# Kernel optimization log

Hardware: AMD Instinct MI355X
Metric: run time of the kernel (lower is better)

Reference implementation:

```python
import jax, jax.numpy as jnp
import numpy as np
from jax import lax

B, KLEN, KDIM, QDIM, ADIM, VDIM = 32, 2000, 512, 512, 512, 512
CONV_CH, CONV_K = 10, 201

def setup_inputs() -> dict:
    key = jax.random.key(0)
    ks = jax.random.split(key, 16)
    s = lambda fan: 1.0 / np.sqrt(fan)
    return {
        "key": jax.random.normal(ks[0], (B, KLEN, KDIM), jnp.float32),
        "value": jax.random.normal(ks[1], (B, KLEN, VDIM), jnp.float32),
        "query": jax.random.normal(ks[2], (B, 1, QDIM), jnp.float32),
        "aw_prev": jnp.zeros((B, 1, KLEN), jnp.float32),
        "mask": jnp.ones((B, 1, KLEN), jnp.int32),
        # parameters (torch nn.Linear: y = x @ W.T + b, W is [out,in])
        "Wk": jax.random.uniform(ks[3], (ADIM, KDIM), jnp.float32, -s(KDIM), s(KDIM)),
        "bk": jax.random.uniform(ks[4], (ADIM,), jnp.float32, -s(KDIM), s(KDIM)),
        "Wq": jax.random.uniform(ks[5], (ADIM, QDIM), jnp.float32, -s(QDIM), s(QDIM)),
        "conv_w": jax.random.uniform(ks[6], (CONV_CH, 1, CONV_K), jnp.float32, -s(CONV_K), s(CONV_K)),
        "Wconv": jax.random.uniform(ks[7], (ADIM, CONV_CH), jnp.float32, -s(CONV_CH), s(CONV_CH)),
        "v": jax.random.uniform(ks[8], (ADIM,), jnp.float32, -s(ADIM), s(ADIM)),
    }

def reference(key, value, query, aw_prev, mask, Wk, bk, Wq, conv_w, Wconv, v):
    # location-aware attention, qlen == 1, sharpening_factor == 1, no dropout (eval)
    kproj = jnp.einsum('bkd,ad->bka', key, Wk) + bk              # [B, klen, adim]
    qproj = jnp.einsum('bqd,ad->bqa', query, Wq)                 # [B, 1, adim]
    # conv over previous attention weights: 1D 'same' conv, 1 -> CONV_CH channels
    conv_feat = lax.conv_general_dilated(
        aw_prev, conv_w, window_strides=(1,), padding='SAME',
        dimension_numbers=('NCH', 'OIH', 'NCH'))                 # [B, C, klen]
    conv_proj = jnp.einsum('bck,ac->bka', conv_feat, Wconv)      # [B, klen, adim]
    # additive score: v^T tanh(Wk k + Wq q + Wc f)
    tmp = jnp.tanh(kproj[:, None] + qproj[:, :, None] + conv_proj[:, None])  # [B,1,klen,adim]
    e = jnp.einsum('bqka,a->bqk', tmp, v)                        # [B, 1, klen]
    neg_inf = jnp.finfo(e.dtype).min
    e = jnp.where(mask == 0, neg_inf, e)
    aw = jax.nn.softmax(e, axis=-1)                              # [B, 1, klen]
    cv = jnp.einsum('bqk,bkv->bqv', aw, value)                   # [B, 1, vdim]
    return cv, aw[:, None]  # aw: [B, 1(H), 1(qlen), klen]
```

## Files before the change

### kernel.cpp

```cpp
#include <hip/hip_runtime.h>
#include <hip/hip_bf16.h>
#include <math.h>

#define B 32
#define KLEN 2000
#define KDIM 512
#define QDIM 512
#define ADIM 512
#define VDIM 512
#define CONV_CH 10
#define CONV_K 201
#define NROWS (B*KLEN)

#define NKS  33
#define ZERO16 {0,0,0,0,0,0,0,0,0,0,0,0,0,0,0,0}

typedef __attribute__((ext_vector_type(8)))  short bf16x8;
typedef __attribute__((ext_vector_type(16))) float f32x16;
typedef __attribute__((ext_vector_type(4)))  float f32x4;
typedef __attribute__((ext_vector_type(2)))  float f32x2;

__device__ __forceinline__ ushort f32_to_bf16(float f) {
    union { float f; unsigned int u; } v; v.f = f;
    unsigned int x = v.u;
    unsigned int r = (x + 0x7FFFu + ((x >> 16) & 1u)) >> 16;
    return (ushort)r;
}

__device__ __forceinline__ float fast_tanh(float x) {
    return 1.0f - 2.0f / (__expf(2.0f * x) + 1.0f);
}

#define MFMA32(a, bfr, c) __builtin_amdgcn_mfma_f32_32x32x16_bf16(a, bfr, c, 0, 0, 0)

__global__ void k_pack_w(const float* __restrict__ Wk, const float* __restrict__ Wconv,
                         const float* __restrict__ bk, ushort* __restrict__ wp) {
    int t = blockIdx.x * 256 + threadIdx.x;
    int lane = t & 63;
    int idx = t >> 6;
    int ks = idx % NKS, nt = idx / NKS;
    int h = lane >> 5, r = lane & 31;
    int a = nt * 32 + r;
    int j0 = ks * 16 + h * 8;
    union { uint4 v; ushort u[8]; } pk;
    #pragma unroll
    for (int jj = 0; jj < 8; jj++) {
        int j = j0 + jj;
        float val;
        if (j < 512)       val = Wk[a * KDIM + j];
        else if (j < 522)  val = Wconv[a * CONV_CH + (j - 512)];
        else if (j == 522) val = bk[a];
        else               val = 0.f;
        pk.u[jj] = f32_to_bf16(val);
    }
    *(uint4*)(wp + (size_t)t * 8) = pk.v;
}

__global__ void k_qproj(const float* __restrict__ query, const float* __restrict__ Wq,
                        float* __restrict__ qproj) {
    int t = blockIdx.x * 256 + threadIdx.x;
    int b = t >> 9, a = t & 511;
    const f32x4* q = (const f32x4*)(query + b * QDIM);
    const f32x4* w = (const f32x4*)(Wq + a * QDIM);
    float acc = 0.f;
    #pragma unroll 4
    for (int i = 0; i < 128; i++) {
        f32x4 qv = q[i], wv = w[i];
        acc += qv[0]*wv[0] + qv[1]*wv[1] + qv[2]*wv[2] + qv[3]*wv[3];
    }
    qproj[t] = acc;
}

__global__ void k_conv(const float* __restrict__ aw_prev, const float* __restrict__ conv_w,
                       float* __restrict__ cf) {
    int t = blockIdx.x * 256 + threadIdx.x;
    if (t >= B * CONV_CH * KLEN) return;
    int k = t % KLEN;
    int c = (t / KLEN) % CONV_CH;
    int b = t / (KLEN * CONV_CH);
    const float* aw = aw_prev + b * KLEN;
    const float* w  = conv_w + c * CONV_K;
    int lo = k - 100;
    int t0 = lo < 0 ? -lo : 0;
    int t1 = (lo + CONV_K > KLEN) ? (KLEN - lo) : CONV_K;
    float acc = 0.f;
    for (int tt = t0; tt < t1; tt++) acc += w[tt] * aw[lo + tt];
    cf[t] = acc;
}

__global__ __launch_bounds__(512, 4)
void k_main(const float* __restrict__ key, const ushort* __restrict__ wp,
            const float* __restrict__ qproj, const float* __restrict__ cf,
            const float* __restrict__ vvec, const int* __restrict__ mask,
            float* __restrict__ e_out) {
    __shared__ char Alds[65536];
    __shared__ float partsum[8][2][32];
    const int tid = threadIdx.x;
    const int wc = tid >> 6, lane = tid & 63;
    const int r = lane & 31, h = lane >> 5;
    const int b = blockIdx.x >> 5;
    const int kbase = (blockIdx.x & 31) * 64;

    #pragma unroll
    for (int i = 0; i < 8; i++) {
        int ch = tid + i * 512;
        int arow = ch >> 6, cx = ch & 63;
        int kpos = kbase + arow; if (kpos >= KLEN) kpos = KLEN - 1;
        const float* kp = key + ((size_t)b * KLEN + kpos) * KDIM + cx * 8;
        f32x4 f0 = __builtin_nontemporal_load((const f32x4*)kp);
        f32x4 f1 = __builtin_nontemporal_load((const f32x4*)(kp + 4));
        union { uint4 v; ushort u[8]; } pk;
        pk.u[0] = f32_to_bf16(f0[0]); pk.u[1] = f32_to_bf16(f0[1]);
        pk.u[2] = f32_to_bf16(f0[2]); pk.u[3] = f32_to_bf16(f0[3]);
        pk.u[4] = f32_to_bf16(f1[0]); pk.u[5] = f32_to_bf16(f1[1]);
        pk.u[6] = f32_to_bf16(f1[2]); pk.u[7] = f32_to_bf16(f1[3]);
        int off = arow * 1024 + cx * 16;
        off ^= (arow & 31) << 4;
        *(uint4*)(Alds + off) = pk.v;
    }
    __syncthreads();

    const ushort* bpW0 = wp + ((size_t)(wc * 2 + 0) * NKS * 64 + lane) * 8;
    const ushort* bpW1 = wp + ((size_t)(wc * 2 + 1) * NKS * 64 + lane) * 8;
    const int base_g0 = r * 1024 + h * 16;
    const int base_g1 = base_g0 + 32768;
    const int swz = r << 4;

    f32x16 c00 = ZERO16, c01 = ZERO16;
    f32x16 c10 = ZERO16, c11 = ZERO16;

    #pragma unroll 4
    for (int ks = 0; ks < 32; ks++) {
        bf16x8 k0 = *(const bf16x8*)(Alds + ((base_g0 + ks * 32) ^ swz));
        bf16x8 k1 = *(const bf16x8*)(Alds + ((base_g1 + ks * 32) ^ swz));
        bf16x8 w0 = *(const bf16x8*)(bpW0 + ks * 512);
        bf16x8 w1 = *(const bf16x8*)(bpW1 + ks * 512);
        c00 = MFMA32(w0, k0, c00); c01 = MFMA32(w0, k1, c01);
        c10 = MFMA32(w1, k0, c10); c11 = MFMA32(w1, k1, c11);
    }
    {
        auto build_ext = [&](int kpos) -> bf16x8 {
            int kc = kpos < KLEN ? kpos : KLEN - 1;
            const float* cfb = cf + ((size_t)b * CONV_CH) * KLEN + kc;
            union { bf16x8 v8; ushort u[8]; } pk;
            if (h == 0) {
                #pragma unroll
                for (int jj = 0; jj < 8; jj++) pk.u[jj] = f32_to_bf16(cfb[(size_t)jj * KLEN]);
            } else {
                pk.u[0] = f32_to_bf16(cfb[(size_t)8 * KLEN]);
                pk.u[1] = f32_to_bf16(cfb[(size_t)9 * KLEN]);
                pk.u[2] = 0x3F80;
                pk.u[3] = 0; pk.u[4] = 0; pk.u[5] = 0; pk.u[6] = 0; pk.u[7] = 0;
            }
            return pk.v8;
        };
        bf16x8 x0 = build_ext(kbase + r);
        bf16x8 x1 = build_ext(kbase + 32 + r);
        bf16x8 w0 = *(const bf16x8*)(bpW0 + 32 * 512);
        bf16x8 w1 = *(const bf16x8*)(bpW1 + 32 * 512);
        c00 = MFMA32(w0, x0, c00); c01 = MFMA32(w0, x1, c01);
        c10 = MFMA32(w1, x0, c10); c11 = MFMA32(w1, x1, c11);
    }

    const float* qb = qproj + b * ADIM + wc * 64;
    const float* vb = vvec + wc * 64;
    float pg0 = 0.f, pg1 = 0.f;
    #pragma unroll
    for (int t = 0; t < 2; t++) {
        const f32x16 a0 = t ? c10 : c00;
        const f32x16 a1 = t ? c11 : c01;
        #pragma unroll
        for (int q = 0; q < 4; q++) {
            f32x4 qv = *(const f32x4*)(qb + t * 32 + 8 * q + 4 * h);
            f32x4 vv = *(const f32x4*)(vb + t * 32 + 8 * q + 4 * h);
            #pragma unroll
            for (int j = 0; j < 4; j++) {
                int i = 4 * q + j;
                pg0 += fast_tanh(a0[i] + qv[j]) * vv[j];
                pg1 += fast_tanh(a1[i] + qv[j]) * vv[j];
            }
        }
    }
    pg0 += __shfl_xor(pg0, 32);
    pg1 += __shfl_xor(pg1, 32);
    if (h == 0) { partsum[wc][0][r] = pg0; partsum[wc][1][r] = pg1; }
    __syncthreads();

    if (tid < 64) {
        int g = tid >> 5, rr = tid & 31;
        float s = 0.f;
        #pragma unroll
        for (int w = 0; w < 8; w++) s += partsum[w][g][rr];
        int kpos = kbase + g * 32 + rr;
        if (kpos < KLEN) {
            int idx = b * KLEN + kpos;
            e_out[idx] = mask[idx] ? s : -3.4028235e38f;
        }
    }
}

__global__ void k_softmax(const float* __restrict__ e, float* __restrict__ aw) {
    int b = blockIdx.x;
    const float* er = e + b * KLEN;
    __shared__ float redm[4], reds[4];
    int tid = threadIdx.x, lane = tid & 63, wv = tid >> 6;
    float m = -3.4028235e38f;
    for (int k = tid; k < KLEN; k += 256) m = fmaxf(m, er[k]);
    for (int o = 32; o; o >>= 1) m = fmaxf(m, __shfl_xor(m, o));
    if (lane == 0) redm[wv] = m;
    __syncthreads();
    m = fmaxf(fmaxf(redm[0], redm[1]), fmaxf(redm[2], redm[3]));
    float s = 0.f;
    for (int k = tid; k < KLEN; k += 256) s += __expf(er[k] - m);
    for (int o = 32; o; o >>= 1) s += __shfl_xor(s, o);
    if (lane == 0) reds[wv] = s;
    __syncthreads();
    s = reds[0] + reds[1] + reds[2] + reds[3];
    float inv = 1.0f / s;
    for (int k = tid; k < KLEN; k += 256) aw[b * KLEN + k] = __expf(er[k] - m) * inv;
}

__global__ void k_cvpart(const float* __restrict__ aw, const float* __restrict__ value,
                         float* __restrict__ part) {
    int b = blockIdx.x >> 3, chunk = blockIdx.x & 7;
    int k0 = chunk * 250;
    __shared__ float sa[256];
    __shared__ f32x4 red[128];
    int tid = threadIdx.x;
    if (tid < 250) sa[tid] = aw[b * KLEN + k0 + tid];
    __syncthreads();
    const int kh = tid >> 7;
    const int col4 = (tid & 127) * 4;
    const float* vp = value + ((size_t)b * KLEN + k0 + kh) * VDIM + col4;
    f32x4 acc = {0.f, 0.f, 0.f, 0.f};
    #pragma unroll 5
    for (int k = 0; k < 250; k += 2) {
        f32x4 vv = __builtin_nontemporal_load((const f32x4*)(vp + (size_t)k * VDIM));
        acc += vv * sa[k + kh];
    }
    if (kh == 1) red[tid & 127] = acc;
    __syncthreads();
    if (kh == 0) {
        acc += red[tid];
        *(f32x4*)(part + ((b * 8 + chunk) * VDIM) + col4) = acc;
    }
}

__global__ void k_cvreduce(const float* __restrict__ part, float* __restrict__ cv) {
    int t = blockIdx.x * 256 + threadIdx.x;
    int b = t >> 9, col = t & 511;
    float s = 0.f;
    #pragma unroll
    for (int c = 0; c < 8; c++) s += part[(b * 8 + c) * VDIM + col];
    cv[t] = s;
}

extern "C" void kernel_launch(void* const* d_in, const int* in_sizes, int n_in,
                              void* d_out, int out_size, void* d_ws, size_t ws_size,
                              hipStream_t stream) {
    const float* key     = (const float*)d_in[0];
    const float* value   = (const float*)d_in[1];
    const float* query   = (const float*)d_in[2];
    const float* aw_prev = (const float*)d_in[3];
    const int*   mask    = (const int*)d_in[4];
    const float* Wk      = (const float*)d_in[5];
    const float* bk      = (const float*)d_in[6];
    const float* Wq      = (const float*)d_in[7];
    const float* conv_w  = (const float*)d_in[8];
    const float* Wconv   = (const float*)d_in[9];
    const float* vvec    = (const float*)d_in[10];

    char* ws = (char*)d_ws;
    ushort* wp   = (ushort*)(ws + 0);
    float* qproj = (float*)(ws + 540672);
    float* cf    = (float*)(ws + 606208);
    float* e     = (float*)(ws + 3166208);
    float* part  = (float*)(ws + 3422208);

    float* cv = (float*)d_out;
    float* aw = (float*)d_out + B * VDIM;

    k_pack_w  <<<132,  256, 0, stream>>>(Wk, Wconv, bk, wp);
    k_qproj   <<<64,   256, 0, stream>>>(query, Wq, qproj);
    k_conv    <<<2500, 256, 0, stream>>>(aw_prev, conv_w, cf);
    k_main    <<<1024, 512, 0, stream>>>(key, wp, qproj, cf, vvec, mask, e);
    k_softmax <<<B,    256, 0, stream>>>(e, aw);
    k_cvpart  <<<B*8,  256, 0, stream>>>(aw, value, part);
    k_cvreduce<<<64,   256, 0, stream>>>(part, cv);
}
```

Baseline: 157.5 us.

## Fuse prep kernels into one launch, tile conv through LDS, widen cv split

```diff
diff --git a/kernel.cpp b/kernel.cpp
--- a/kernel.cpp
+++ b/kernel.cpp
@@ -15,6 +15,10 @@
 #define NKS  33
 #define ZERO16 {0,0,0,0,0,0,0,0,0,0,0,0,0,0,0,0}
 
+#define NP_PACK 53
+#define NP_QPRJ 26
+#define NP_CONV 256
+
 typedef __attribute__((ext_vector_type(8)))  short bf16x8;
 typedef __attribute__((ext_vector_type(16))) float f32x16;
 typedef __attribute__((ext_vector_type(4)))  float f32x4;
@@ -33,59 +37,94 @@
 
 #define MFMA32(a, bfr, c) __builtin_amdgcn_mfma_f32_32x32x16_bf16(a, bfr, c, 0, 0, 0)
 
-__global__ void k_pack_w(const float* __restrict__ Wk, const float* __restrict__ Wconv,
-                         const float* __restrict__ bk, ushort* __restrict__ wp) {
-    int t = blockIdx.x * 256 + threadIdx.x;
-    int lane = t & 63;
-    int idx = t >> 6;
-    int ks = idx % NKS, nt = idx / NKS;
-    int h = lane >> 5, r = lane & 31;
-    int a = nt * 32 + r;
-    int j0 = ks * 16 + h * 8;
-    union { uint4 v; ushort u[8]; } pk;
-    #pragma unroll
-    for (int jj = 0; jj < 8; jj++) {
-        int j = j0 + jj;
-        float val;
-        if (j < 512)       val = Wk[a * KDIM + j];
-        else if (j < 522)  val = Wconv[a * CONV_CH + (j - 512)];
-        else if (j == 522) val = bk[a];
-        else               val = 0.f;
-        pk.u[jj] = f32_to_bf16(val);
-    }
-    *(uint4*)(wp + (size_t)t * 8) = pk.v;
-}
-
-__global__ void k_qproj(const float* __restrict__ query, const float* __restrict__ Wq,
-                        float* __restrict__ qproj) {
-    int t = blockIdx.x * 256 + threadIdx.x;
-    int b = t >> 9, a = t & 511;
-    const f32x4* q = (const f32x4*)(query + b * QDIM);
-    const f32x4* w = (const f32x4*)(Wq + a * QDIM);
-    float acc = 0.f;
-    #pragma unroll 4
-    for (int i = 0; i < 128; i++) {
-        f32x4 qv = q[i], wv = w[i];
-        acc += qv[0]*wv[0] + qv[1]*wv[1] + qv[2]*wv[2] + qv[3]*wv[3];
-    }
-    qproj[t] = acc;
-}
-
-__global__ void k_conv(const float* __restrict__ aw_prev, const float* __restrict__ conv_w,
-                       float* __restrict__ cf) {
-    int t = blockIdx.x * 256 + threadIdx.x;
-    if (t >= B * CONV_CH * KLEN) return;
-    int k = t % KLEN;
-    int c = (t / KLEN) % CONV_CH;
-    int b = t / (KLEN * CONV_CH);
-    const float* aw = aw_prev + b * KLEN;
-    const float* w  = conv_w + c * CONV_K;
-    int lo = k - 100;
-    int t0 = lo < 0 ? -lo : 0;
-    int t1 = (lo + CONV_K > KLEN) ? (KLEN - lo) : CONV_K;
-    float acc = 0.f;
-    for (int tt = t0; tt < t1; tt++) acc += w[tt] * aw[lo + tt];
-    cf[t] = acc;
+__global__ __launch_bounds__(640, 2)
+void k_prep(const float* __restrict__ Wk, const float* __restrict__ Wconv,
+            const float* __restrict__ bk, ushort* __restrict__ wp,
+            const float* __restrict__ query, const float* __restrict__ Wq,
+            float* __restrict__ qproj,
+            const float* __restrict__ aw_prev, const float* __restrict__ conv_w,
+            float* __restrict__ cf) {
+    __shared__ float w_s[CONV_CH * 204];
+    __shared__ float aw_s[464];
+    const int bid = blockIdx.x, tid = threadIdx.x;
+
+    if (bid < NP_PACK) {
+        int t = bid * 640 + tid;
+        if (t < 16 * NKS * 64) {
+            int lane = t & 63;
+            int idx = t >> 6;
+            int ks = idx % NKS, nt = idx / NKS;
+            int h = lane >> 5, r = lane & 31;
+            int a = nt * 32 + r;
+            int j0 = ks * 16 + h * 8;
+            union { uint4 v; ushort u[8]; } pk;
+            #pragma unroll
+            for (int jj = 0; jj < 8; jj++) {
+                int j = j0 + jj;
+                float val;
+                if (j < 512)       val = Wk[a * KDIM + j];
+                else if (j < 522)  val = Wconv[a * CONV_CH + (j - 512)];
+                else if (j == 522) val = bk[a];
+                else               val = 0.f;
+                pk.u[jj] = f32_to_bf16(val);
+            }
+            *(uint4*)(wp + (size_t)t * 8) = pk.v;
+        }
+    } else if (bid < NP_PACK + NP_QPRJ) {
+        int t = (bid - NP_PACK) * 640 + tid;
+        if (t < B * ADIM) {
+            int b = t >> 9, a = t & 511;
+            const f32x4* q = (const f32x4*)(query + b * QDIM);
+            const f32x4* w = (const f32x4*)(Wq + a * QDIM);
+            float acc = 0.f;
+            #pragma unroll 4
+            for (int i = 0; i < 128; i++) {
+                f32x4 qv = q[i], wv = w[i];
+                acc += qv[0]*wv[0] + qv[1]*wv[1] + qv[2]*wv[2] + qv[3]*wv[3];
+            }
+            qproj[t] = acc;
+        }
+    } else {
+        int cb = bid - NP_PACK - NP_QPRJ;
+        int b = cb >> 3, chunk = cb & 7;
+        int k0 = chunk * 256;
+        for (int i = tid; i < CONV_CH * 204; i += 640) {
+            int c = i / 204, t = i % 204;
+            w_s[i] = (t < CONV_K) ? conv_w[c * CONV_K + t] : 0.f;
+        }
+        for (int i = tid; i < 464; i += 640) {
+            int src = k0 - 100 + i;
+            aw_s[i] = (src >= 0 && src < KLEN) ? aw_prev[b * KLEN + src] : 0.f;
+        }
+        __syncthreads();
+
+        const int c = tid >> 6;
+        const int k_local = (tid & 63) * 4;
+        const float* wc = w_s + c * 204;
+        float a0 = 0.f, a1 = 0.f, a2 = 0.f, a3 = 0.f;
+        f32x4 r0 = *(const f32x4*)(aw_s + k_local);
+        #pragma unroll 3
+        for (int q = 0; q < 51; q++) {
+            f32x4 r1 = *(const f32x4*)(aw_s + k_local + 4 * q + 4);
+            float w0 = wc[4*q], w1 = wc[4*q+1], w2 = wc[4*q+2], w3 = wc[4*q+3];
+            a0 += w0*r0[0]; a1 += w0*r0[1]; a2 += w0*r0[2]; a3 += w0*r0[3];
+            a0 += w1*r0[1]; a1 += w1*r0[2]; a2 += w1*r0[3]; a3 += w1*r1[0];
+            a0 += w2*r0[2]; a1 += w2*r0[3]; a2 += w2*r1[0]; a3 += w2*r1[1];
+            a0 += w3*r0[3]; a1 += w3*r1[0]; a2 += w3*r1[1]; a3 += w3*r1[2];
+            r0 = r1;
+        }
+        int k = k0 + k_local;
+        float* dst = cf + ((size_t)b * CONV_CH + c) * KLEN + k;
+        if (k + 3 < KLEN) {
+            f32x4 o; o[0] = a0; o[1] = a1; o[2] = a2; o[3] = a3;
+            *(f32x4*)dst = o;
+        } else {
+            if (k     < KLEN) dst[0] = a0;
+            if (k + 1 < KLEN) dst[1] = a1;
+            if (k + 2 < KLEN) dst[2] = a2;
+            if (k + 3 < KLEN) dst[3] = a3;
+        }
+    }
 }
 
 __global__ __launch_bounds__(512, 4)
@@ -220,29 +259,29 @@
     for (int k = tid; k < KLEN; k += 256) aw[b * KLEN + k] = __expf(er[k] - m) * inv;
 }
 
-__global__ void k_cvpart(const float* __restrict__ aw, const float* __restrict__ value,
-                         float* __restrict__ part) {
-    int b = blockIdx.x >> 3, chunk = blockIdx.x & 7;
-    int k0 = chunk * 250;
-    __shared__ float sa[256];
-    __shared__ f32x4 red[128];
+__global__ __launch_bounds__(512, 2)
+void k_cvpart(const float* __restrict__ aw, const float* __restrict__ value,
+              float* __restrict__ part) {
+    int b = blockIdx.x >> 4, chunk = blockIdx.x & 15;
+    int k0 = chunk * 125;
+    __shared__ float sa[128];
+    __shared__ f32x4 red[3][128];
     int tid = threadIdx.x;
-    if (tid < 250) sa[tid] = aw[b * KLEN + k0 + tid];
+    if (tid < 125) sa[tid] = aw[b * KLEN + k0 + tid];
     __syncthreads();
     const int kh = tid >> 7;
-    const int col4 = (tid & 127) * 4;
-    const float* vp = value + ((size_t)b * KLEN + k0 + kh) * VDIM + col4;
+    const int colt = tid & 127;
+    const float* vp = value + ((size_t)b * KLEN + k0) * VDIM + colt * 4;
     f32x4 acc = {0.f, 0.f, 0.f, 0.f};
-    #pragma unroll 5
-    for (int k = 0; k < 250; k += 2) {
+    for (int k = kh; k < 125; k += 4) {
         f32x4 vv = __builtin_nontemporal_load((const f32x4*)(vp + (size_t)k * VDIM));
-        acc += vv * sa[k + kh];
-    }
-    if (kh == 1) red[tid & 127] = acc;
+        acc += vv * sa[k];
+    }
+    if (kh) red[kh - 1][colt] = acc;
     __syncthreads();
     if (kh == 0) {
-        acc += red[tid];
-        *(f32x4*)(part + ((b * 8 + chunk) * VDIM) + col4) = acc;
+        acc += red[0][colt] + red[1][colt] + red[2][colt];
+        *(f32x4*)(part + ((b * 16 + chunk) * VDIM) + colt * 4) = acc;
     }
 }
 
@@ -251,7 +290,7 @@
     int b = t >> 9, col = t & 511;
     float s = 0.f;
     #pragma unroll
-    for (int c = 0; c < 8; c++) s += part[(b * 8 + c) * VDIM + col];
+    for (int c = 0; c < 16; c++) s += part[(b * 16 + c) * VDIM + col];
     cv[t] = s;
 }
 
@@ -280,11 +319,10 @@
     float* cv = (float*)d_out;
     float* aw = (float*)d_out + B * VDIM;
 
-    k_pack_w  <<<132,  256, 0, stream>>>(Wk, Wconv, bk, wp);
-    k_qproj   <<<64,   256, 0, stream>>>(query, Wq, qproj);
-    k_conv    <<<2500, 256, 0, stream>>>(aw_prev, conv_w, cf);
+    k_prep    <<<NP_PACK + NP_QPRJ + NP_CONV, 640, 0, stream>>>(
+                  Wk, Wconv, bk, wp, query, Wq, qproj, aw_prev, conv_w, cf);
     k_main    <<<1024, 512, 0, stream>>>(key, wp, qproj, cf, vvec, mask, e);
     k_softmax <<<B,    256, 0, stream>>>(e, aw);
-    k_cvpart  <<<B*8,  256, 0, stream>>>(aw, value, part);
+    k_cvpart  <<<B*16, 512, 0, stream>>>(aw, value, part);
     k_cvreduce<<<64,   256, 0, stream>>>(part, cv);
 }
```

Measured after the change: 142.7 us. -9.3%, faster.
